# Performance work log

Hardware: AMD Instinct MI355X
Metric: run time of the kernel (lower is better)

Reference implementation:

```python
import jax, jax.numpy as jnp
import numpy as np

N = 50000      # nodes
E = 400000     # edges (before self loops)
IN = 128       # in_channels
H = 4          # num_heads (layers 1-2)
C = 32         # hidden_dim per head
HID = H * C    # 128 total hidden
CLS = 40       # num_classes (out_heads = 1)
EPS = 1e-5     # BatchNorm eps
SLOPE = 0.2    # LeakyReLU negative slope (PyG GATConv default)


def setup_inputs() -> dict:
    key = jax.random.key(0)
    ks = jax.random.split(key, 24)
    rn = lambda k, shp, s: jax.random.normal(k, shp, jnp.float32) * s
    x = jax.random.normal(ks[0], (N, IN), jnp.float32)
    src = jax.random.randint(ks[1], (E,), 0, N)
    dst = jax.random.randint(ks[2], (E,), 0, N)
    src = jnp.where(src == dst, (src + 1) % N, src)  # no pre-existing self loops
    edge_index = jnp.stack([src, dst]).astype(jnp.int32)
    inp = dict(x=x, edge_index=edge_index)
    # conv1: in IN -> H heads x C
    inp['W1'] = rn(ks[3], (IN, H * C), 1.0 / np.sqrt(IN))
    inp['as1'] = rn(ks[4], (H, C), 0.1)
    inp['ad1'] = rn(ks[5], (H, C), 0.1)
    inp['b1'] = rn(ks[6], (H * C,), 0.02)
    # conv2: HID -> H x C
    inp['W2'] = rn(ks[7], (HID, H * C), 1.0 / np.sqrt(HID))
    inp['as2'] = rn(ks[8], (H, C), 0.1)
    inp['ad2'] = rn(ks[9], (H, C), 0.1)
    inp['b2'] = rn(ks[10], (H * C,), 0.02)
    # conv3: HID -> 1 head x CLS, concat=False
    inp['W3'] = rn(ks[11], (HID, CLS), 1.0 / np.sqrt(HID))
    inp['as3'] = rn(ks[12], (1, CLS), 0.1)
    inp['ad3'] = rn(ks[13], (1, CLS), 0.1)
    inp['b3'] = rn(ks[14], (CLS,), 0.02)
    # residual projection
    inp['Wres'] = rn(ks[15], (IN, HID), 1.0 / np.sqrt(IN))
    # BatchNorm (eval mode: running stats)
    inp['g1'] = 1.0 + rn(ks[16], (HID,), 0.1)
    inp['be1'] = rn(ks[17], (HID,), 0.1)
    inp['m1'] = rn(ks[18], (HID,), 0.1)
    inp['v1'] = 1.0 + jax.random.uniform(ks[19], (HID,), jnp.float32) * 0.5
    inp['g2'] = 1.0 + rn(ks[20], (HID,), 0.1)
    inp['be2'] = rn(ks[21], (HID,), 0.1)
    inp['m2'] = rn(ks[22], (HID,), 0.1)
    inp['v2'] = 1.0 + jax.random.uniform(ks[23], (HID,), jnp.float32) * 0.5
    return inp


def _gat_conv(h, src, dst, W, a_src, a_dst, bias, heads, out_ch, concat):
    """PyG-style GATConv (eval: attention dropout off), self loops already in src/dst."""
    n = h.shape[0]
    xw = (h @ W).reshape(n, heads, out_ch)                    # [N,H,C]
    e_src = jnp.sum(xw * a_src, axis=-1)                      # [N,H]
    e_dst = jnp.sum(xw * a_dst, axis=-1)                      # [N,H]
    e = jax.nn.leaky_relu(e_src[src] + e_dst[dst], SLOPE)     # [E',H]
    # segment softmax over incoming edges of each dst node
    mseg = jax.ops.segment_max(e, dst, num_segments=n)        # [N,H]
    ex = jnp.exp(e - mseg[dst])
    den = jax.ops.segment_sum(ex, dst, num_segments=n)
    alpha = ex / den[dst]                                     # [E',H]
    out = jax.ops.segment_sum(alpha[:, :, None] * xw[src], dst, num_segments=n)  # [N,H,C]
    out = out.reshape(n, heads * out_ch) if concat else out.mean(axis=1)
    return out + bias


def _bn(h, g, b, m, v):
    return (h - m) * jax.lax.rsqrt(v + EPS) * g + b


def reference(x, edge_index, W1, as1, ad1, b1, W2, as2, ad2, b2,
              W3, as3, ad3, b3, Wres, g1, be1, m1, v1, g2, be2, m2, v2):
    n = x.shape[0]
    loop = jnp.arange(n, dtype=edge_index.dtype)
    src = jnp.concatenate([edge_index[0], loop])  # add self loops (PyG default)
    dst = jnp.concatenate([edge_index[1], loop])
    x0 = x
    h = _gat_conv(x0, src, dst, W1, as1, ad1, b1, H, C, True)
    h = jax.nn.elu(_bn(h, g1, be1, m1, v1) + x0 @ Wres)
    h_res = h
    h = _gat_conv(h, src, dst, W2, as2, ad2, b2, H, C, True)
    h = jax.nn.elu(_bn(h, g2, be2, m2, v2) + h_res)
    logits = _gat_conv(h, src, dst, W3, as3, ad3, b3, 1, CLS, False)
    return logits
```

## Files before the change

kernel.cpp:

```cpp
#include <hip/hip_runtime.h>
#include <hip/hip_bf16.h>

#define THREADS 256

typedef __attribute__((ext_vector_type(8))) short bfrag;
typedef __attribute__((ext_vector_type(4))) float f32x4;

__device__ inline unsigned short f2b(float v) {
    __hip_bfloat16 b = __float2bfloat16(v);
    return *reinterpret_cast<unsigned short*>(&b);
}
__device__ inline float b2f(unsigned short u) {
    return __uint_as_float(((unsigned)u) << 16);
}
__device__ inline float rdv(const void* p, int off, bool isbf) {
    return isbf ? b2f(((const unsigned short*)p)[off]) : ((const float*)p)[off];
}

__global__ void detect_kernel(const unsigned short* __restrict__ x, int n, int* flag) {
    __shared__ int cnt;
    if (threadIdx.x == 0) cnt = 0;
    __syncthreads();
    int local = 0;
    for (int i = threadIdx.x; i < n; i += THREADS) {
        unsigned ex = (x[i] >> 7) & 0xFF;
        if (ex == 0xFF || ex >= 134 || (ex > 0 && ex <= 100)) local++;
    }
    atomicAdd(&cnt, local);
    __syncthreads();
    if (threadIdx.x == 0) *flag = (cnt * 8 > n) ? 0 : 1;
}

struct InPtrs { const void* p[23]; };

__global__ void prep_kernel(InPtrs in, const int* __restrict__ flag,
                            unsigned short* __restrict__ Wl1, unsigned short* __restrict__ Wl2,
                            unsigned short* __restrict__ WlR, unsigned short* __restrict__ Wl3,
                            float* __restrict__ bnsc1, float* __restrict__ bnsh1,
                            float* __restrict__ bnsc2, float* __restrict__ bnsh2,
                            float* __restrict__ AS1f, float* __restrict__ AD1f,
                            float* __restrict__ AS2f, float* __restrict__ AD2f,
                            float* __restrict__ AS3f, float* __restrict__ AD3f,
                            float* __restrict__ B3f, unsigned short* __restrict__ xb, int N) {
    bool isbf = (*flag != 0);
    int b = blockIdx.x;
    if (b < 27) {
        const void* Wv; unsigned short* o; int cols, tt;
        if (b < 8)       { Wv = in.p[2];  o = Wl1; cols = 128; tt = b; }
        else if (b < 16) { Wv = in.p[6];  o = Wl2; cols = 128; tt = b - 8; }
        else if (b < 24) { Wv = in.p[14]; o = WlR; cols = 128; tt = b - 16; }
        else             { Wv = in.p[10]; o = Wl3; cols = 40;  tt = b - 24; }
        int id = tt * 256 + threadIdx.x;
        int t = id >> 8, ks = (id >> 6) & 3, l = id & 63;
        int q = l >> 4, n = l & 15;
        int c = t * 16 + n;
#pragma unroll
        for (int j = 0; j < 8; ++j) {
            int k = ks * 32 + q * 8 + j;
            float v = (c < cols) ? rdv(Wv, k * cols + c, isbf) : 0.f;
            o[id * 8 + j] = f2b(v);
        }
    } else if (b == 27) {
        int c = threadIdx.x;
        if (c < 128) {
            float s = rdv(in.p[15], c, isbf) * rsqrtf(rdv(in.p[18], c, isbf) + 1e-5f);
            bnsc1[c] = s;
            bnsh1[c] = rdv(in.p[16], c, isbf) - rdv(in.p[17], c, isbf) * s +
                       rdv(in.p[5], c, isbf) * s;
            AS1f[c] = rdv(in.p[3], c, isbf);
            AD1f[c] = rdv(in.p[4], c, isbf);
            AS2f[c] = rdv(in.p[7], c, isbf);
            AD2f[c] = rdv(in.p[8], c, isbf);
        } else {
            int d = c - 128;
            float s = rdv(in.p[19], d, isbf) * rsqrtf(rdv(in.p[22], d, isbf) + 1e-5f);
            bnsc2[d] = s;
            bnsh2[d] = rdv(in.p[20], d, isbf) - rdv(in.p[21], d, isbf) * s +
                       rdv(in.p[9], d, isbf) * s;
            if (d < 40) {
                AS3f[d] = rdv(in.p[11], d, isbf);
                AD3f[d] = rdv(in.p[12], d, isbf);
                B3f[d] = rdv(in.p[13], d, isbf);
            }
        }
    } else {
        if (isbf) return;
        const float* xf = (const float*)in.p[0];
        int total = N * 128;
        int stride = (gridDim.x - 28) * 256;
        for (int i = (b - 28) * 256 + threadIdx.x; i < total; i += stride) xb[i] = f2b(xf[i]);
    }
}

__global__ void count_kernel(const int* __restrict__ ei, int* __restrict__ deg, int E, int N) {
    int e = blockIdx.x * THREADS + threadIdx.x;
    if (e >= E + N) return;
    int d = (e < E) ? ei[E + e] : (e - E);
    atomicAdd(&deg[d], 1);
}

__global__ void bsum_kernel(const int* __restrict__ deg, int* __restrict__ bsum, int N) {
    int idx = blockIdx.x * 256 + threadIdx.x;
    int lane = threadIdx.x & 63, wv = threadIdx.x >> 6;
    int v = (idx < N) ? deg[idx] : 0;
#pragma unroll
    for (int o = 1; o < 64; o <<= 1) v += __shfl_xor(v, o, 64);
    __shared__ int ws[4];
    if (lane == 0) ws[wv] = v;
    __syncthreads();
    if (threadIdx.x == 0) bsum[blockIdx.x] = ws[0] + ws[1] + ws[2] + ws[3];
}

__global__ __launch_bounds__(1024) void bscan_kernel(const int* __restrict__ bsum,
                                                     int* __restrict__ boff, int nb) {
    __shared__ int ws[16];
    int tid = threadIdx.x, lane = tid & 63, wv = tid >> 6;
    int v = (tid < nb) ? bsum[tid] : 0;
    int sc = v;
#pragma unroll
    for (int o = 1; o < 64; o <<= 1) {
        int t = __shfl_up(sc, o, 64);
        if (lane >= o) sc += t;
    }
    if (lane == 63) ws[wv] = sc;
    __syncthreads();
    int add = 0;
#pragma unroll
    for (int k = 0; k < 16; ++k) add += (k < wv) ? ws[k] : 0;
    if (tid < nb) boff[tid] = add + sc - v;
}

__global__ void scanw_kernel(const int* __restrict__ deg, const int* __restrict__ boff,
                             int* __restrict__ row_ptr, int* __restrict__ pos, int N) {
    int idx = blockIdx.x * 256 + threadIdx.x;
    int lane = threadIdx.x & 63, wv = threadIdx.x >> 6;
    int v = (idx < N) ? deg[idx] : 0;
    int sc = v;
#pragma unroll
    for (int o = 1; o < 64; o <<= 1) {
        int t = __shfl_up(sc, o, 64);
        if (lane >= o) sc += t;
    }
    __shared__ int ws[4];
    if (lane == 63) ws[wv] = sc;
    __syncthreads();
    int add = boff[blockIdx.x];
#pragma unroll
    for (int k = 0; k < 4; ++k) add += (k < wv) ? ws[k] : 0;
    int excl = add + sc - v;
    if (idx < N) {
        pos[idx] = excl;
        row_ptr[idx + 1] = excl + v;
    }
    if (idx == 0) row_ptr[0] = 0;
}

__global__ void scatter_kernel(const int* __restrict__ ei, int* __restrict__ pos,
                               int* __restrict__ csr, int E, int N) {
    int e = blockIdx.x * THREADS + threadIdx.x;
    if (e >= E + N) return;
    int s, d;
    if (e < E) { s = ei[e]; d = ei[E + e]; }
    else { s = e - E; d = s; }
    int p = atomicAdd(&pos[d], 1);
    csr[p] = s;
}

template <int COLT, int HEADS, bool ES>
__global__ __launch_bounds__(256) void gemm_mfma(
    const unsigned short* __restrict__ A, const unsigned short* __restrict__ Wg,
    const float* __restrict__ as_f, const float* __restrict__ ad_f,
    unsigned short* __restrict__ out, int ldc, int cols,
    float* __restrict__ es, float* __restrict__ ed, int N) {
    __shared__ __align__(16) unsigned short Wls[COLT * 2048];
    int tid = threadIdx.x;
    {
        const float4* src = (const float4*)Wg;
        float4* dst = (float4*)Wls;
#pragma unroll
        for (int i = 0; i < COLT; ++i) dst[tid + i * 256] = src[tid + i * 256];
    }
    __syncthreads();
    int w = tid >> 6, lane = tid & 63;
    int n = lane & 15, q = lane >> 4;
    int row0 = blockIdx.x * 64 + w * 16;
    int ar = row0 + n; ar = ar < N ? ar : N - 1;
    f32x4 acc[COLT];
#pragma unroll
    for (int t = 0; t < COLT; ++t) acc[t] = (f32x4){0.f, 0.f, 0.f, 0.f};
    const unsigned short* arow = A + (size_t)ar * 128;
#pragma unroll
    for (int ks = 0; ks < 4; ++ks) {
        bfrag a = *reinterpret_cast<const bfrag*>(arow + ks * 32 + q * 8);
#pragma unroll
        for (int t = 0; t < COLT; ++t) {
            bfrag b = *reinterpret_cast<const bfrag*>(&Wls[((t * 4 + ks) * 64 + lane) * 8]);
            acc[t] = __builtin_amdgcn_mfma_f32_16x16x32_bf16(a, b, acc[t], 0, 0, 0);
        }
    }
    if (ES) {
        float asv[COLT], adv[COLT];
#pragma unroll
        for (int t = 0; t < COLT; ++t) {
            int c = t * 16 + n;
            asv[t] = (c < cols) ? as_f[c] : 0.f;
            adv[t] = (c < cols) ? ad_f[c] : 0.f;
        }
#pragma unroll
        for (int r = 0; r < 4; ++r) {
            float pe[HEADS], pd[HEADS];
#pragma unroll
            for (int h = 0; h < HEADS; ++h) { pe[h] = 0.f; pd[h] = 0.f; }
#pragma unroll
            for (int t = 0; t < COLT; ++t) {
                int h = (HEADS == 4) ? (t >> 1) : 0;
                pe[h] = fmaf(acc[t][r], asv[t], pe[h]);
                pd[h] = fmaf(acc[t][r], adv[t], pd[h]);
            }
#pragma unroll
            for (int h = 0; h < HEADS; ++h) {
#pragma unroll
                for (int o = 1; o < 16; o <<= 1) {
                    pe[h] += __shfl_xor(pe[h], o, 64);
                    pd[h] += __shfl_xor(pd[h], o, 64);
                }
            }
            int row = row0 + q * 4 + r;
            if (n == 0 && row < N) {
#pragma unroll
                for (int h = 0; h < HEADS; ++h) {
                    es[(size_t)row * HEADS + h] = pe[h];
                    ed[(size_t)row * HEADS + h] = pd[h];
                }
            }
        }
    }
#pragma unroll
    for (int t = 0; t < COLT; ++t) {
        int col = t * 16 + n;
        if (col < cols) {
#pragma unroll
            for (int r = 0; r < 4; ++r) {
                int row = row0 + q * 4 + r;
                if (row < N) out[(size_t)row * ldc + col] = f2b(acc[t][r]);
            }
        }
    }
}

__global__ __launch_bounds__(256) void gemm_dual(
    const unsigned short* __restrict__ Araw, const unsigned short* __restrict__ Acvt,
    const int* __restrict__ flag,
    const unsigned short* __restrict__ Wg1, const unsigned short* __restrict__ WgR,
    const float* __restrict__ as_f, const float* __restrict__ ad_f,
    unsigned short* __restrict__ xwb, unsigned short* __restrict__ resb,
    float* __restrict__ es, float* __restrict__ ed, int N) {
    __shared__ __align__(16) unsigned short Wls[16 * 2048];
    int tid = threadIdx.x;
    {
        const float4* s1 = (const float4*)Wg1;
        const float4* s2 = (const float4*)WgR;
        float4* dst = (float4*)Wls;
#pragma unroll
        for (int i = 0; i < 8; ++i) dst[tid + i * 256] = s1[tid + i * 256];
#pragma unroll
        for (int i = 0; i < 8; ++i) dst[2048 + tid + i * 256] = s2[tid + i * 256];
    }
    const unsigned short* A = (*flag) ? Araw : Acvt;
    __syncthreads();
    int w = tid >> 6, lane = tid & 63;
    int n = lane & 15, q = lane >> 4;
    int row0 = blockIdx.x * 64 + w * 16;
    int ar = row0 + n; ar = ar < N ? ar : N - 1;
    f32x4 acc[16];
#pragma unroll
    for (int t = 0; t < 16; ++t) acc[t] = (f32x4){0.f, 0.f, 0.f, 0.f};
    const unsigned short* arow = A + (size_t)ar * 128;
#pragma unroll
    for (int ks = 0; ks < 4; ++ks) {
        bfrag a = *reinterpret_cast<const bfrag*>(arow + ks * 32 + q * 8);
#pragma unroll
        for (int t = 0; t < 8; ++t) {
            bfrag b = *reinterpret_cast<const bfrag*>(&Wls[((t * 4 + ks) * 64 + lane) * 8]);
            acc[t] = __builtin_amdgcn_mfma_f32_16x16x32_bf16(a, b, acc[t], 0, 0, 0);
        }
#pragma unroll
        for (int t = 0; t < 8; ++t) {
            bfrag b = *reinterpret_cast<const bfrag*>(&Wls[16384 + ((t * 4 + ks) * 64 + lane) * 8]);
            acc[8 + t] = __builtin_amdgcn_mfma_f32_16x16x32_bf16(a, b, acc[8 + t], 0, 0, 0);
        }
    }
    float asv[8], adv[8];
#pragma unroll
    for (int t = 0; t < 8; ++t) {
        int c = t * 16 + n;
        asv[t] = as_f[c];
        adv[t] = ad_f[c];
    }
#pragma unroll
    for (int r = 0; r < 4; ++r) {
        float pe[4] = {0.f, 0.f, 0.f, 0.f}, pd[4] = {0.f, 0.f, 0.f, 0.f};
#pragma unroll
        for (int t = 0; t < 8; ++t) {
            int h = t >> 1;
            pe[h] = fmaf(acc[t][r], asv[t], pe[h]);
            pd[h] = fmaf(acc[t][r], adv[t], pd[h]);
        }
#pragma unroll
        for (int h = 0; h < 4; ++h) {
#pragma unroll
            for (int o = 1; o < 16; o <<= 1) {
                pe[h] += __shfl_xor(pe[h], o, 64);
                pd[h] += __shfl_xor(pd[h], o, 64);
            }
        }
        int row = row0 + q * 4 + r;
        if (n == 0 && row < N) {
#pragma unroll
            for (int h = 0; h < 4; ++h) {
                es[(size_t)row * 4 + h] = pe[h];
                ed[(size_t)row * 4 + h] = pd[h];
            }
        }
    }
#pragma unroll
    for (int t = 0; t < 8; ++t) {
        int col = t * 16 + n;
#pragma unroll
        for (int r = 0; r < 4; ++r) {
            int row = row0 + q * 4 + r;
            if (row < N) {
                xwb[(size_t)row * 128 + col] = f2b(acc[t][r]);
                resb[(size_t)row * 128 + col] = f2b(acc[8 + t][r]);
            }
        }
    }
}

__global__ __launch_bounds__(256) void agg128_fused(
    const unsigned short* __restrict__ xwb, const float* __restrict__ es,
    const float* __restrict__ ed, const int* __restrict__ row_ptr,
    const int* __restrict__ csr, const float* __restrict__ bnsc,
    const float* __restrict__ bnsh, const unsigned short* __restrict__ resb,
    unsigned short* __restrict__ outb, int N) {
    int w = threadIdx.x >> 6, lane = threadIdx.x & 63;
    int node = blockIdx.x * 4 + w;
    if (node >= N) return;
    int h = lane >> 4;
    int i16 = lane & 15;
    int base = lane & 48;
    int c0 = lane * 2;
    float edl = ed[node * 4 + h];
    int start = row_ptr[node], end = row_ptr[node + 1];
    float den = 0.f, a0 = 0.f, a1 = 0.f;
    for (int jb = start; jb < end; jb += 16) {
        int cnt = end - jb; cnt = cnt < 16 ? cnt : 16;
        int sv = csr[jb + (i16 < cnt ? i16 : 0)];
        unsigned uu[16];
#pragma unroll
        for (int u = 0; u < 16; ++u) {
            int s = __shfl(sv, u, 64);
            uu[u] = *(const unsigned*)(xwb + (size_t)s * 128 + c0);
        }
        float wgl = 0.f;
        if (i16 < cnt) {
            float e = es[sv * 4 + h] + edl;
            e = e > 0.f ? e : 0.2f * e;
            wgl = __expf(e);
        }
        float d = wgl;
        d += __shfl_xor(d, 1, 64);
        d += __shfl_xor(d, 2, 64);
        d += __shfl_xor(d, 4, 64);
        d += __shfl_xor(d, 8, 64);
        den += d;
#pragma unroll
        for (int u = 0; u < 16; ++u) {
            float wg = __shfl(wgl, base + u, 64);
            a0 = fmaf(wg, __uint_as_float(uu[u] << 16), a0);
            a1 = fmaf(wg, __uint_as_float(uu[u] & 0xffff0000u), a1);
        }
    }
    float inv = 1.f / den;
    float2 sc = *(const float2*)(bnsc + c0);
    float2 sh = *(const float2*)(bnsh + c0);
    unsigned ur = *(const unsigned*)(resb + (size_t)node * 128 + c0);
    float v0 = fmaf(a0 * inv, sc.x, sh.x) + __uint_as_float(ur << 16);
    float v1 = fmaf(a1 * inv, sc.y, sh.y) + __uint_as_float(ur & 0xffff0000u);
    v0 = v0 > 0.f ? v0 : expm1f(v0);
    v1 = v1 > 0.f ? v1 : expm1f(v1);
    unsigned pk = (unsigned)f2b(v0) | ((unsigned)f2b(v1) << 16);
    *(unsigned*)(outb + (size_t)node * 128 + c0) = pk;
}

__global__ __launch_bounds__(256) void agg40_kernel(
    const unsigned short* __restrict__ xw3b, const float* __restrict__ es3,
    const float* __restrict__ ed3, const int* __restrict__ row_ptr,
    const int* __restrict__ csr, const float* __restrict__ b3,
    void* __restrict__ out, const int* __restrict__ flag, int N) {
    int w = threadIdx.x >> 6, lane = threadIdx.x & 63;
    int node = blockIdx.x * 4 + w;
    if (node >= N) return;
    int i16 = lane & 15;
    int g = lane >= 40 ? 2 : (lane >= 20 ? 1 : 0);
    int cp = lane - g * 20;
    int c0 = cp * 2; c0 = c0 > 38 ? 38 : c0;
    float edl = ed3[node];
    int start = row_ptr[node], end = row_ptr[node + 1];
    float den = 0.f, a0 = 0.f, a1 = 0.f;
    for (int jb = start; jb < end; jb += 16) {
        int cnt = end - jb; cnt = cnt < 16 ? cnt : 16;
        int sv = csr[jb + (i16 < cnt ? i16 : 0)];
        unsigned uu[6];
#pragma unroll
        for (int t = 0; t < 6; ++t) {
            int slot = 3 * t + g; slot = slot < 15 ? slot : 15;
            int s = __shfl(sv, slot, 64);
            uu[t] = *(const unsigned*)(xw3b + (size_t)s * 40 + c0);
        }
        float wgl = 0.f;
        if (i16 < cnt) {
            float e = es3[sv] + edl;
            e = e > 0.f ? e : 0.2f * e;
            wgl = __expf(e);
        }
        float d = wgl;
        d += __shfl_xor(d, 1, 64);
        d += __shfl_xor(d, 2, 64);
        d += __shfl_xor(d, 4, 64);
        d += __shfl_xor(d, 8, 64);
        den += d;
#pragma unroll
        for (int t = 0; t < 6; ++t) {
            int slot = 3 * t + g;
            int sl = slot < 15 ? slot : 15;
            float wg = __shfl(wgl, sl, 64);
            if (slot >= cnt) wg = 0.f;
            a0 = fmaf(wg, __uint_as_float(uu[t] << 16), a0);
            a1 = fmaf(wg, __uint_as_float(uu[t] & 0xffff0000u), a1);
        }
    }
    float t0 = __shfl(a0, (lane + 20) & 63, 64);
    float t1 = __shfl(a0, (lane + 40) & 63, 64);
    float u0 = __shfl(a1, (lane + 20) & 63, 64);
    float u1 = __shfl(a1, (lane + 40) & 63, 64);
    a0 += t0 + t1;
    a1 += u0 + u1;
    if (lane < 20) {
        float inv = 1.f / den;
        float v0 = a0 * inv + b3[c0];
        float v1 = a1 * inv + b3[c0 + 1];
        size_t eoff = (size_t)node * 40 + c0;
        if (*flag) {
            unsigned pk = (unsigned)f2b(v0) | ((unsigned)f2b(v1) << 16);
            *(unsigned*)((unsigned short*)out + eoff) = pk;
        } else {
            *(float2*)((float*)out + eoff) = make_float2(v0, v1);
        }
    }
}

extern "C" void kernel_launch(void* const* d_in, const int* in_sizes, int n_in,
                              void* d_out, int out_size, void* d_ws, size_t ws_size,
                              hipStream_t stream) {
    (void)n_in; (void)out_size; (void)ws_size;
    const int N = in_sizes[0] / 128;
    const int E = in_sizes[1] / 2;
    const int EPN = E + N;
    const int NB = (N + 255) / 256;
    char* base = (char*)d_ws;
    size_t off = 0;
    auto alloc = [&](size_t bytes) -> char* {
        char* p = base + off;
        off = (off + bytes + 255) & ~(size_t)255;
        return p;
    };
    int* flag = (int*)alloc(4);
    int* deg = (int*)alloc((size_t)N * 4);
    int* row_ptr = (int*)alloc((size_t)(N + 1) * 4);
    int* pos = (int*)alloc((size_t)N * 4);
    int* bsum = (int*)alloc((size_t)NB * 4);
    int* boff = (int*)alloc((size_t)NB * 4);
    int* csr = (int*)alloc((size_t)EPN * 4);
    float* bnsc1 = (float*)alloc(512); float* bnsh1 = (float*)alloc(512);
    float* bnsc2 = (float*)alloc(512); float* bnsh2 = (float*)alloc(512);
    float* AS1f = (float*)alloc(512); float* AD1f = (float*)alloc(512);
    float* AS2f = (float*)alloc(512); float* AD2f = (float*)alloc(512);
    float* AS3f = (float*)alloc(256); float* AD3f = (float*)alloc(256);
    float* B3f = (float*)alloc(256);
    unsigned short* Wl1 = (unsigned short*)alloc(32768);
    unsigned short* Wl2 = (unsigned short*)alloc(32768);
    unsigned short* WlR = (unsigned short*)alloc(32768);
    unsigned short* Wl3 = (unsigned short*)alloc(12288);
    unsigned short* xb = (unsigned short*)alloc((size_t)N * 128 * 2);
    unsigned short* xwb = (unsigned short*)alloc((size_t)N * 128 * 2);
    unsigned short* h1b = (unsigned short*)alloc((size_t)N * 128 * 2);
    unsigned short* resb = (unsigned short*)alloc((size_t)N * 128 * 2);
    float* es = (float*)alloc((size_t)N * 4 * 4);
    float* ed = (float*)alloc((size_t)N * 4 * 4);

    const int* ei = (const int*)d_in[1];

    hipMemsetAsync(deg, 0, (size_t)N * 4, stream);
    detect_kernel<<<1, THREADS, 0, stream>>>((const unsigned short*)d_in[0], 4096, flag);

    InPtrs ip;
    for (int t = 0; t < 23; t++) ip.p[t] = d_in[t];
    prep_kernel<<<28 + 2048, THREADS, 0, stream>>>(ip, flag, Wl1, Wl2, WlR, Wl3,
                                                   bnsc1, bnsh1, bnsc2, bnsh2,
                                                   AS1f, AD1f, AS2f, AD2f,
                                                   AS3f, AD3f, B3f, xb, N);

    count_kernel<<<(EPN + THREADS - 1) / THREADS, THREADS, 0, stream>>>(ei, deg, E, N);
    bsum_kernel<<<NB, 256, 0, stream>>>(deg, bsum, N);
    bscan_kernel<<<1, 1024, 0, stream>>>(bsum, boff, NB);
    scanw_kernel<<<NB, 256, 0, stream>>>(deg, boff, row_ptr, pos, N);
    scatter_kernel<<<(EPN + THREADS - 1) / THREADS, THREADS, 0, stream>>>(ei, pos, csr, E, N);

    int gemmGrid = (N + 63) / 64;
    int aggGrid = (N + 3) / 4;

    gemm_dual<<<gemmGrid, 256, 0, stream>>>((const unsigned short*)d_in[0], xb, flag,
                                            Wl1, WlR, AS1f, AD1f, xwb, resb, es, ed, N);
    agg128_fused<<<aggGrid, 256, 0, stream>>>(xwb, es, ed, row_ptr, csr,
                                              bnsc1, bnsh1, resb, h1b, N);
    gemm_mfma<8, 4, true><<<gemmGrid, 256, 0, stream>>>(
        h1b, Wl2, AS2f, AD2f, xwb, 128, 128, es, ed, N);
    unsigned short* h2b = resb;
    agg128_fused<<<aggGrid, 256, 0, stream>>>(xwb, es, ed, row_ptr, csr,
                                              bnsc2, bnsh2, h1b, h2b, N);
    gemm_mfma<3, 1, true><<<gemmGrid, 256, 0, stream>>>(
        h2b, Wl3, AS3f, AD3f, xwb, 40, 40, es, ed, N);
    agg40_kernel<<<aggGrid, 256, 0, stream>>>(xwb, es, ed, row_ptr, csr, B3f, d_out, flag, N);
}
```

Before: 300.6 us.

## Use head-blocked feature layout with per-head aggregation passes and fold degree counting into prep

Features and attention scores are stored head-major, as [head][node][32] and [head][node], so each aggregation pass over one head touches a 3.2MB slice that can stay cache-resident. The aggregation kernels now give each 16- or 20-lane group its own node and walk edges one at a time with a prefetched next index, instead of shuffling batches of 16 neighbors. Degree counting is merged into the prep kernel to drop a launch. The trade-off is four passes over the CSR and serial per-edge dependency chains with less memory-level parallelism per lane.

```diff
diff --git a/kernel.cpp b/kernel.cpp
--- a/kernel.cpp
+++ b/kernel.cpp
@@ -41,7 +41,9 @@
                             float* __restrict__ AS1f, float* __restrict__ AD1f,
                             float* __restrict__ AS2f, float* __restrict__ AD2f,
                             float* __restrict__ AS3f, float* __restrict__ AD3f,
-                            float* __restrict__ B3f, unsigned short* __restrict__ xb, int N) {
+                            float* __restrict__ B3f, unsigned short* __restrict__ xb,
+                            int N, const int* __restrict__ ei, int* __restrict__ deg,
+                            int E, int CB) {
     bool isbf = (*flag != 0);
     int b = blockIdx.x;
     if (b < 27) {
@@ -83,20 +85,20 @@
                 B3f[d] = rdv(in.p[13], d, isbf);
             }
         }
+    } else if (b < 28 + CB) {
+        int i = (b - 28) * 256 + threadIdx.x;
+        if (i < E + N) {
+            int d = (i < E) ? ei[E + i] : (i - E);
+            atomicAdd(&deg[d], 1);
+        }
     } else {
         if (isbf) return;
         const float* xf = (const float*)in.p[0];
         int total = N * 128;
-        int stride = (gridDim.x - 28) * 256;
-        for (int i = (b - 28) * 256 + threadIdx.x; i < total; i += stride) xb[i] = f2b(xf[i]);
-    }
-}
-
-__global__ void count_kernel(const int* __restrict__ ei, int* __restrict__ deg, int E, int N) {
-    int e = blockIdx.x * THREADS + threadIdx.x;
-    if (e >= E + N) return;
-    int d = (e < E) ? ei[E + e] : (e - E);
-    atomicAdd(&deg[d], 1);
+        int stride = (gridDim.x - 28 - CB) * 256;
+        for (int i = (b - 28 - CB) * 256 + threadIdx.x; i < total; i += stride)
+            xb[i] = f2b(xf[i]);
+    }
 }
 
 __global__ void bsum_kernel(const int* __restrict__ deg, int* __restrict__ bsum, int N) {
@@ -166,12 +168,13 @@
     csr[p] = s;
 }
 
-template <int COLT, int HEADS, bool ES>
+template <int COLT, int HEADS, bool ES, bool CBLK>
 __global__ __launch_bounds__(256) void gemm_mfma(
     const unsigned short* __restrict__ A, const unsigned short* __restrict__ Wg,
     const float* __restrict__ as_f, const float* __restrict__ ad_f,
     unsigned short* __restrict__ out, int ldc, int cols,
-    float* __restrict__ es, float* __restrict__ ed, int N) {
+    float* __restrict__ es, float* __restrict__ ed, int N,
+    long aRow, long aKs) {
     __shared__ __align__(16) unsigned short Wls[COLT * 2048];
     int tid = threadIdx.x;
     {
@@ -188,10 +191,10 @@
     f32x4 acc[COLT];
 #pragma unroll
     for (int t = 0; t < COLT; ++t) acc[t] = (f32x4){0.f, 0.f, 0.f, 0.f};
-    const unsigned short* arow = A + (size_t)ar * 128;
+    const unsigned short* abase = A + (size_t)ar * aRow;
 #pragma unroll
     for (int ks = 0; ks < 4; ++ks) {
-        bfrag a = *reinterpret_cast<const bfrag*>(arow + ks * 32 + q * 8);
+        bfrag a = *reinterpret_cast<const bfrag*>(abase + (size_t)ks * aKs + q * 8);
 #pragma unroll
         for (int t = 0; t < COLT; ++t) {
             bfrag b = *reinterpret_cast<const bfrag*>(&Wls[((t * 4 + ks) * 64 + lane) * 8]);
@@ -229,8 +232,8 @@
             if (n == 0 && row < N) {
 #pragma unroll
                 for (int h = 0; h < HEADS; ++h) {
-                    es[(size_t)row * HEADS + h] = pe[h];
-                    ed[(size_t)row * HEADS + h] = pd[h];
+                    es[(size_t)h * N + row] = pe[h];
+                    ed[(size_t)h * N + row] = pd[h];
                 }
             }
         }
@@ -242,7 +245,13 @@
 #pragma unroll
             for (int r = 0; r < 4; ++r) {
                 int row = row0 + q * 4 + r;
-                if (row < N) out[(size_t)row * ldc + col] = f2b(acc[t][r]);
+                if (row < N) {
+                    if (CBLK)
+                        out[(size_t)(col >> 5) * N * 32 + (size_t)row * 32 + (col & 31)] =
+                            f2b(acc[t][r]);
+                    else
+                        out[(size_t)row * ldc + col] = f2b(acc[t][r]);
+                }
             }
         }
     }
@@ -318,8 +327,8 @@
         if (n == 0 && row < N) {
 #pragma unroll
             for (int h = 0; h < 4; ++h) {
-                es[(size_t)row * 4 + h] = pe[h];
-                ed[(size_t)row * 4 + h] = pd[h];
+                es[(size_t)h * N + row] = pe[h];
+                ed[(size_t)h * N + row] = pd[h];
             }
         }
     }
@@ -330,67 +339,65 @@
         for (int r = 0; r < 4; ++r) {
             int row = row0 + q * 4 + r;
             if (row < N) {
-                xwb[(size_t)row * 128 + col] = f2b(acc[t][r]);
-                resb[(size_t)row * 128 + col] = f2b(acc[8 + t][r]);
-            }
-        }
-    }
-}
-
-__global__ __launch_bounds__(256) void agg128_fused(
+                size_t o = (size_t)(col >> 5) * N * 32 + (size_t)row * 32 + (col & 31);
+                xwb[o] = f2b(acc[t][r]);
+                resb[o] = f2b(acc[8 + t][r]);
+            }
+        }
+    }
+}
+
+__global__ __launch_bounds__(256) void agg128_mp(
     const unsigned short* __restrict__ xwb, const float* __restrict__ es,
     const float* __restrict__ ed, const int* __restrict__ row_ptr,
     const int* __restrict__ csr, const float* __restrict__ bnsc,
     const float* __restrict__ bnsh, const unsigned short* __restrict__ resb,
-    unsigned short* __restrict__ outb, int N) {
+    unsigned short* __restrict__ outb, int N, int nb) {
+    int pass = blockIdx.x / nb;
+    int blk = blockIdx.x - pass * nb;
     int w = threadIdx.x >> 6, lane = threadIdx.x & 63;
-    int node = blockIdx.x * 4 + w;
-    if (node >= N) return;
-    int h = lane >> 4;
-    int i16 = lane & 15;
-    int base = lane & 48;
-    int c0 = lane * 2;
-    float edl = ed[node * 4 + h];
-    int start = row_ptr[node], end = row_ptr[node + 1];
+    int grp = lane >> 4, l16 = lane & 15;
+    int node = blk * 16 + w * 4 + grp;
+    bool act = node < N;
+    int start = 0, end = 0;
+    float edl = 0.f;
+    if (act) {
+        start = row_ptr[node];
+        end = row_ptr[node + 1];
+        edl = ed[(size_t)pass * N + node];
+    }
+    const unsigned short* xh = xwb + (size_t)pass * N * 32;
+    const float* esh = es + (size_t)pass * N;
     float den = 0.f, a0 = 0.f, a1 = 0.f;
-    for (int jb = start; jb < end; jb += 16) {
-        int cnt = end - jb; cnt = cnt < 16 ? cnt : 16;
-        int sv = csr[jb + (i16 < cnt ? i16 : 0)];
-        unsigned uu[16];
-#pragma unroll
-        for (int u = 0; u < 16; ++u) {
-            int s = __shfl(sv, u, 64);
-            uu[u] = *(const unsigned*)(xwb + (size_t)s * 128 + c0);
-        }
-        float wgl = 0.f;
-        if (i16 < cnt) {
-            float e = es[sv * 4 + h] + edl;
-            e = e > 0.f ? e : 0.2f * e;
-            wgl = __expf(e);
-        }
-        float d = wgl;
-        d += __shfl_xor(d, 1, 64);
-        d += __shfl_xor(d, 2, 64);
-        d += __shfl_xor(d, 4, 64);
-        d += __shfl_xor(d, 8, 64);
-        den += d;
-#pragma unroll
-        for (int u = 0; u < 16; ++u) {
-            float wg = __shfl(wgl, base + u, 64);
-            a0 = fmaf(wg, __uint_as_float(uu[u] << 16), a0);
-            a1 = fmaf(wg, __uint_as_float(uu[u] & 0xffff0000u), a1);
-        }
-    }
-    float inv = 1.f / den;
-    float2 sc = *(const float2*)(bnsc + c0);
-    float2 sh = *(const float2*)(bnsh + c0);
-    unsigned ur = *(const unsigned*)(resb + (size_t)node * 128 + c0);
-    float v0 = fmaf(a0 * inv, sc.x, sh.x) + __uint_as_float(ur << 16);
-    float v1 = fmaf(a1 * inv, sc.y, sh.y) + __uint_as_float(ur & 0xffff0000u);
-    v0 = v0 > 0.f ? v0 : expm1f(v0);
-    v1 = v1 > 0.f ? v1 : expm1f(v1);
-    unsigned pk = (unsigned)f2b(v0) | ((unsigned)f2b(v1) << 16);
-    *(unsigned*)(outb + (size_t)node * 128 + c0) = pk;
+    int j = start;
+    int sv = (j < end) ? csr[j] : 0;
+    while (j < end) {
+        int svn = (j + 1 < end) ? csr[j + 1] : 0;
+        unsigned uu = *(const unsigned*)(xh + (size_t)sv * 32 + l16 * 2);
+        float e = esh[sv] + edl;
+        e = e > 0.f ? e : 0.2f * e;
+        float wg = __expf(e);
+        den += wg;
+        a0 = fmaf(wg, __uint_as_float(uu << 16), a0);
+        a1 = fmaf(wg, __uint_as_float(uu & 0xffff0000u), a1);
+        sv = svn;
+        ++j;
+    }
+    if (act) {
+        int c0 = l16 * 2;
+        int cg = pass * 32 + c0;
+        float inv = 1.f / den;
+        float2 sc = *(const float2*)(bnsc + cg);
+        float2 sh = *(const float2*)(bnsh + cg);
+        size_t ro = (size_t)pass * N * 32 + (size_t)node * 32 + c0;
+        unsigned ur = *(const unsigned*)(resb + ro);
+        float v0 = fmaf(a0 * inv, sc.x, sh.x) + __uint_as_float(ur << 16);
+        float v1 = fmaf(a1 * inv, sc.y, sh.y) + __uint_as_float(ur & 0xffff0000u);
+        v0 = v0 > 0.f ? v0 : expm1f(v0);
+        v1 = v1 > 0.f ? v1 : expm1f(v1);
+        unsigned pk = (unsigned)f2b(v0) | ((unsigned)f2b(v1) << 16);
+        *(unsigned*)(outb + ro) = pk;
+    }
 }
 
 __global__ __launch_bounds__(256) void agg40_kernel(
@@ -399,54 +406,35 @@
     const int* __restrict__ csr, const float* __restrict__ b3,
     void* __restrict__ out, const int* __restrict__ flag, int N) {
     int w = threadIdx.x >> 6, lane = threadIdx.x & 63;
-    int node = blockIdx.x * 4 + w;
-    if (node >= N) return;
-    int i16 = lane & 15;
-    int g = lane >= 40 ? 2 : (lane >= 20 ? 1 : 0);
-    int cp = lane - g * 20;
-    int c0 = cp * 2; c0 = c0 > 38 ? 38 : c0;
-    float edl = ed3[node];
-    int start = row_ptr[node], end = row_ptr[node + 1];
+    int grp = lane < 20 ? 0 : (lane < 40 ? 1 : 2);
+    int l20 = lane - grp * 20;
+    bool act = (lane < 60);
+    int node = (blockIdx.x * 4 + w) * 3 + grp;
+    if (node >= N) act = false;
+    int start = 0, end = 0;
+    float edl = 0.f;
+    if (act) {
+        start = row_ptr[node];
+        end = row_ptr[node + 1];
+        edl = ed3[node];
+    }
+    int c0 = l20 * 2;
     float den = 0.f, a0 = 0.f, a1 = 0.f;
-    for (int jb = start; jb < end; jb += 16) {
-        int cnt = end - jb; cnt = cnt < 16 ? cnt : 16;
-        int sv = csr[jb + (i16 < cnt ? i16 : 0)];
-        unsigned uu[6];
-#pragma unroll
-        for (int t = 0; t < 6; ++t) {
-            int slot = 3 * t + g; slot = slot < 15 ? slot : 15;
-            int s = __shfl(sv, slot, 64);
-            uu[t] = *(const unsigned*)(xw3b + (size_t)s * 40 + c0);
-        }
-        float wgl = 0.f;
-        if (i16 < cnt) {
-            float e = es3[sv] + edl;
-            e = e > 0.f ? e : 0.2f * e;
-            wgl = __expf(e);
-        }
-        float d = wgl;
-        d += __shfl_xor(d, 1, 64);
-        d += __shfl_xor(d, 2, 64);
-        d += __shfl_xor(d, 4, 64);
-        d += __shfl_xor(d, 8, 64);
-        den += d;
-#pragma unroll
-        for (int t = 0; t < 6; ++t) {
-            int slot = 3 * t + g;
-            int sl = slot < 15 ? slot : 15;
-            float wg = __shfl(wgl, sl, 64);
-            if (slot >= cnt) wg = 0.f;
-            a0 = fmaf(wg, __uint_as_float(uu[t] << 16), a0);
-            a1 = fmaf(wg, __uint_as_float(uu[t] & 0xffff0000u), a1);
-        }
-    }
-    float t0 = __shfl(a0, (lane + 20) & 63, 64);
-    float t1 = __shfl(a0, (lane + 40) & 63, 64);
-    float u0 = __shfl(a1, (lane + 20) & 63, 64);
-    float u1 = __shfl(a1, (lane + 40) & 63, 64);
-    a0 += t0 + t1;
-    a1 += u0 + u1;
-    if (lane < 20) {
+    int j = start;
+    int sv = (j < end) ? csr[j] : 0;
+    while (j < end) {
+        int svn = (j + 1 < end) ? csr[j + 1] : 0;
+        unsigned uu = *(const unsigned*)(xw3b + (size_t)sv * 40 + c0);
+        float e = es3[sv] + edl;
+        e = e > 0.f ? e : 0.2f * e;
+        float wg = __expf(e);
+        den += wg;
+        a0 = fmaf(wg, __uint_as_float(uu << 16), a0);
+        a1 = fmaf(wg, __uint_as_float(uu & 0xffff0000u), a1);
+        sv = svn;
+        ++j;
+    }
+    if (act) {
         float inv = 1.f / den;
         float v0 = a0 * inv + b3[c0];
         float v1 = a1 * inv + b3[c0 + 1];
@@ -468,6 +456,7 @@
     const int E = in_sizes[1] / 2;
     const int EPN = E + N;
     const int NB = (N + 255) / 256;
+    const int CB = (EPN + 255) / 256;
     char* base = (char*)d_ws;
     size_t off = 0;
     auto alloc = [&](size_t bytes) -> char* {
@@ -506,30 +495,31 @@
 
     InPtrs ip;
     for (int t = 0; t < 23; t++) ip.p[t] = d_in[t];
-    prep_kernel<<<28 + 2048, THREADS, 0, stream>>>(ip, flag, Wl1, Wl2, WlR, Wl3,
-                                                   bnsc1, bnsh1, bnsc2, bnsh2,
-                                                   AS1f, AD1f, AS2f, AD2f,
-                                                   AS3f, AD3f, B3f, xb, N);
-
-    count_kernel<<<(EPN + THREADS - 1) / THREADS, THREADS, 0, stream>>>(ei, deg, E, N);
+    prep_kernel<<<28 + CB + 2048, THREADS, 0, stream>>>(ip, flag, Wl1, Wl2, WlR, Wl3,
+                                                        bnsc1, bnsh1, bnsc2, bnsh2,
+                                                        AS1f, AD1f, AS2f, AD2f,
+                                                        AS3f, AD3f, B3f, xb, N, ei, deg, E, CB);
+
     bsum_kernel<<<NB, 256, 0, stream>>>(deg, bsum, N);
     bscan_kernel<<<1, 1024, 0, stream>>>(bsum, boff, NB);
     scanw_kernel<<<NB, 256, 0, stream>>>(deg, boff, row_ptr, pos, N);
     scatter_kernel<<<(EPN + THREADS - 1) / THREADS, THREADS, 0, stream>>>(ei, pos, csr, E, N);
 
     int gemmGrid = (N + 63) / 64;
-    int aggGrid = (N + 3) / 4;
+    int nb16 = (N + 15) / 16;
+    int agg40Grid = (N + 11) / 12;
 
     gemm_dual<<<gemmGrid, 256, 0, stream>>>((const unsigned short*)d_in[0], xb, flag,
                                             Wl1, WlR, AS1f, AD1f, xwb, resb, es, ed, N);
-    agg128_fused<<<aggGrid, 256, 0, stream>>>(xwb, es, ed, row_ptr, csr,
-                                              bnsc1, bnsh1, resb, h1b, N);
-    gemm_mfma<8, 4, true><<<gemmGrid, 256, 0, stream>>>(
-        h1b, Wl2, AS2f, AD2f, xwb, 128, 128, es, ed, N);
+    agg128_mp<<<4 * nb16, 256, 0, stream>>>(xwb, es, ed, row_ptr, csr,
+                                            bnsc1, bnsh1, resb, h1b, N, nb16);
+    gemm_mfma<8, 4, true, true><<<gemmGrid, 256, 0, stream>>>(
+        h1b, Wl2, AS2f, AD2f, xwb, 128, 128, es, ed, N, 32L, (long)N * 32);
     unsigned short* h2b = resb;
-    agg128_fused<<<aggGrid, 256, 0, stream>>>(xwb, es, ed, row_ptr, csr,
-                                              bnsc2, bnsh2, h1b, h2b, N);
-    gemm_mfma<3, 1, true><<<gemmGrid, 256, 0, stream>>>(
-        h2b, Wl3, AS3f, AD3f, xwb, 40, 40, es, ed, N);
-    agg40_kernel<<<aggGrid, 256, 0, stream>>>(xwb, es, ed, row_ptr, csr, B3f, d_out, flag, N);
-}
+    agg128_mp<<<4 * nb16, 256, 0, stream>>>(xwb, es, ed, row_ptr, csr,
+                                            bnsc2, bnsh2, h1b, h2b, N, nb16);
+    gemm_mfma<3, 1, true, false><<<gemmGrid, 256, 0, stream>>>(
+        h2b, Wl3, AS3f, AD3f, xwb, 40, 40, es, ed, N, 32L, (long)N * 32);
+    agg40_kernel<<<agg40Grid, 256, 0, stream>>>(xwb, es, ed, row_ptr, csr, B3f,
+                                                d_out, flag, N);
+}
```

Measured after the change: 359.2 us. 1.19x slower.
